# Kernel optimization log

Hardware: AMD Instinct MI355X
Metric: run time of the kernel (lower is better)

Reference implementation:

```python
import jax, jax.numpy as jnp
import numpy as np

B, S, D_IN, D_H = 4, 2048, 1024, 1024


def setup_inputs() -> dict:
    key = jax.random.key(0)
    k1, k2, k3, k4, k5, k6 = jax.random.split(key, 6)
    seq1 = jax.random.normal(k1, (B, S, D_IN), dtype=jnp.float32)
    seq2 = jax.random.normal(k2, (B, S, D_IN), dtype=jnp.float32)
    attn_mask = jax.random.randint(k3, (B, S, S), 0, 2).astype(jnp.bool_)
    # nn.Linear weights: shape [out, in], y = x @ W^T
    scale = 1.0 / np.sqrt(D_IN)
    Wq = jax.random.uniform(k4, (D_H, D_IN), dtype=jnp.float32, minval=-scale, maxval=scale)
    Wk = jax.random.uniform(k5, (D_H, D_IN), dtype=jnp.float32, minval=-scale, maxval=scale)
    Wv = jax.random.uniform(k6, (D_H, D_IN), dtype=jnp.float32, minval=-scale, maxval=scale)
    return {"seq1": seq1, "seq2": seq2, "attn_mask": attn_mask, "Wq": Wq, "Wk": Wk, "Wv": Wv}


def reference(seq1, seq2, attn_mask, Wq, Wk, Wv):
    q = jnp.einsum('bsd,hd->bsh', seq1, Wq)
    k = jnp.einsum('bsd,hd->bsh', seq2, Wk)
    v = jnp.einsum('bsd,hd->bsh', seq2, Wv)
    score = jnp.einsum('bqh,bkh->bqk', q, k) / jnp.sqrt(jnp.float32(q.shape[-1]))
    # faithful to torch.masked_fill(..., value=1e-09): masked positions set to 1e-9
    mask_score = jnp.where(attn_mask, jnp.float32(1e-09), score)
    # faithful to torch.softmax(..., dim=1): softmax over the QUERY axis
    score_matrix = jax.nn.softmax(mask_score, axis=1)
    out = jnp.einsum('bqk,bkh->bqh', score_matrix, v)
    return out
```

## Files before the change

### kernel.cpp

```cpp
#include <hip/hip_runtime.h>

typedef __bf16 bx8 __attribute__((ext_vector_type(8)));
typedef __bf16 bx4 __attribute__((ext_vector_type(4)));
typedef float  fx4 __attribute__((ext_vector_type(4)));
typedef unsigned long long u64;
typedef unsigned char u8;

#define B_   4
#define S_   2048
#define DIN  1024
#define DH   1024

#define MB ((size_t)1 << 20)
#define WS_A1 ((size_t)0)
#define WS_A2 ((size_t)16*MB)
#define WS_PU ((size_t)0)
#define WS_WQ ((size_t)32*MB)
#define WS_BM ((size_t)38*MB)
#define WS_Q  ((size_t)40*MB)
#define WS_K  ((size_t)56*MB)
#define WS_VT ((size_t)72*MB)
#define WS_CS ((size_t)88*MB)

__global__ void prep(const float* __restrict__ s1, const float* __restrict__ s2,
                     const float* __restrict__ wq, const float* __restrict__ wk,
                     const float* __restrict__ wv, const int* __restrict__ mask,
                     __bf16* __restrict__ o1, __bf16* __restrict__ o2,
                     __bf16* __restrict__ ow, u8* __restrict__ bm) {
  const int b = blockIdx.x;
  if (b < 9728) {
    const float* in;
    __bf16* out;
    size_t i;
    if (b < 8192) {
      in  = b < 4096 ? s1 : s2;
      out = b < 4096 ? o1 : o2;
      i = (size_t)(b & 4095) * 256 + threadIdx.x;
    } else {
      int g = b - 8192;
      in  = g < 512 ? wq : (g < 1024 ? wk : wv);
      out = ow + (size_t)(g >> 9) * (DH * DIN);
      i = (size_t)(g & 511) * 256 + threadIdx.x;
    }
    fx4 lo = ((const fx4*)in)[2 * i];
    fx4 hi = ((const fx4*)in)[2 * i + 1];
    bx8 o;
#pragma unroll
    for (int j = 0; j < 4; j++) { o[j] = (__bf16)lo[j]; o[j + 4] = (__bf16)hi[j]; }
    ((bx8*)out)[i] = o;
  } else {
    const int g = b - 9728;
    const int tid = threadIdx.x;
#pragma unroll
    for (int i = 0; i < 8; i++) {
      const int4* mp = (const int4*)mask + (((size_t)g * 16384 + (size_t)i * 2048) >> 2) + tid * 2;
      int4 v0 = mp[0], v1 = mp[1];
      unsigned byte = 0;
      byte |= (v0.x != 0);
      byte |= (v0.y != 0) << 1;
      byte |= (v0.z != 0) << 2;
      byte |= (v0.w != 0) << 3;
      byte |= (v1.x != 0) << 4;
      byte |= (v1.y != 0) << 5;
      byte |= (v1.z != 0) << 6;
      byte |= (v1.w != 0) << 7;
      bm[(size_t)g * 2048 + i * 256 + tid] = (u8)byte;
    }
  }
}


enum { EP_QKV = 0, EP_EXP = 2, EP_F32 = 3 };

#define GLD(gp, lp)                                                              \
  __builtin_amdgcn_global_load_lds(                                              \
      (const __attribute__((address_space(1))) void*)(const void*)(gp),          \
      (__attribute__((address_space(3))) void*)(void*)(lp), 16, 0, 0)

#define ENDSYNC()                                          \
  do {                                                     \
    asm volatile("s_waitcnt vmcnt(0)" ::: "memory");       \
    __builtin_amdgcn_s_barrier();                          \
    __builtin_amdgcn_sched_barrier(0);                     \
  } while (0)

#define MM(m, n, av, bv) \
  acc[m][n] = __builtin_amdgcn_mfma_f32_16x16x32_bf16(av, bv, acc[m][n], 0, 0, 0)

#define LDA_(bo, m, kk) (*(const bx8*)(aBase + (bo) + (m) * 2048 + ((kk) ? c1s : c0s)))
#define LDB_(bo, n, kk) (*(const bx8*)(bBase + (bo) + (n) * 2048 + ((kk) ? c1s : c0s)))

#define STAGE_A(kt, bo) do {                                              \
  GLD(pA + (kt),                    smem + (bo) + tid * 16);              \
  GLD(pA + (size_t)64 * K + (kt),   smem + (bo) + 8192 + tid * 16);       \
} while (0)
#define STAGE_B(kt, bo) do {                                              \
  GLD(pB + (kt),                    smem + (bo) + 16384 + tid * 16);      \
  GLD(pB + (size_t)64 * K + (kt),   smem + (bo) + 24576 + tid * 16);      \
} while (0)

template <int EPI>
__global__ __launch_bounds__(512, 4) void gemm128(
    const __bf16* __restrict__ A, const __bf16* __restrict__ Bm,
    void* __restrict__ Cout, void* __restrict__ Cout2,
    const void* __restrict__ Xtra, int N, int K, long sA, long sB) {
  extern __shared__ char smem[];

  int brow, bcol, bz = 0, qrow = 0;
  bool isQ = false;
  if (EPI == EP_QKV) {
    int f = (blockIdx.x & 7) * 192 + (blockIdx.x >> 3);
    if (f < 512) {
      isQ = true;
      qrow = (f >> 3) * 128;
      brow = qrow;
      bcol = (f & 7) * 128;
    } else {
      int g = f - 512;
      qrow = (g >> 4) * 128;
      brow = 8192 + qrow;
      bcol = (g & 15) * 128;
    }
  } else {
    const unsigned gx = gridDim.x, gy = gridDim.y;
    const unsigned nwg = gx * gy * gridDim.z;
    unsigned flat = (blockIdx.z * gy + blockIdx.y) * gx + blockIdx.x;
    flat = (flat & 7) * (nwg >> 3) + (flat >> 3);
    const int lx = __builtin_ctz(gx), ly = __builtin_ctz(gy);
    brow = ((flat >> lx) & (gy - 1)) * 128;
    bcol = (flat & (gx - 1)) * 128;
    bz   = flat >> (lx + ly);
    A  += (long)bz * sA;
    Bm += (long)bz * sB;
  }

  const int tid  = threadIdx.x;
  const int wid  = tid >> 6;
  const int lane = tid & 63;
  const int wr = wid >> 2;
  const int wc = wid & 3;

  fx4 acc[4][2] = {};

  const int gcol = (((tid & 7) ^ ((tid >> 3) & 7)) << 3);
  const __bf16* Bsel = (EPI == EP_QKV && !isQ) ? (Bm + (size_t)1048576) : Bm;
  const __bf16* pA = A    + (size_t)(brow + (tid >> 3)) * K + gcol;
  const __bf16* pB = Bsel + (size_t)(bcol + (tid >> 3)) * K + gcol;

  const int frow = lane & 15;
  const int slot = (lane >> 4) << 4;
  const int c0s  = slot ^ ((frow & 7) << 4);
  const int c1s  = (64 + slot) ^ ((frow & 7) << 4);
  const char* aBase = smem + (wr * 64 + frow) * 128;
  const char* bBase = smem + 16384 + (wc * 32 + frow) * 128;

  STAGE_A(0, 0); STAGE_B(0, 0);
  ENDSYNC();

  const int nt = K >> 6;
  int cur = 0, nb = 32768;
  bx8 a00, a01, a02, a03, a10, a11, a12, a13, b00, b01, b10, b11;

  for (int t = 0; t < nt; ++t) {
    const int k1 = (t + 1 < nt) ? (t + 1) * 64 : 0;

    STAGE_A(k1, nb); STAGE_B(k1, nb);

    a00 = LDA_(cur, 0, 0); a01 = LDA_(cur, 1, 0); a02 = LDA_(cur, 2, 0); a03 = LDA_(cur, 3, 0);
    b00 = LDB_(cur, 0, 0); b01 = LDB_(cur, 1, 0);
    a10 = LDA_(cur, 0, 1); a11 = LDA_(cur, 1, 1); a12 = LDA_(cur, 2, 1); a13 = LDA_(cur, 3, 1);
    b10 = LDB_(cur, 0, 1); b11 = LDB_(cur, 1, 1);

    __builtin_amdgcn_s_setprio(1);
    MM(0, 0, a00, b00); MM(0, 1, a00, b01);
    MM(1, 0, a01, b00); MM(1, 1, a01, b01);
    MM(2, 0, a02, b00); MM(2, 1, a02, b01);
    MM(3, 0, a03, b00); MM(3, 1, a03, b01);
    MM(0, 0, a10, b10); MM(0, 1, a10, b11);
    MM(1, 0, a11, b10); MM(1, 1, a11, b11);
    MM(2, 0, a12, b10); MM(2, 1, a12, b11);
    MM(3, 0, a13, b10); MM(3, 1, a13, b11);
    __builtin_amdgcn_s_setprio(0);

    ENDSYNC();
    int tmp = cur; cur = nb; nb = tmp;
  }

  const int r0 = wr * 64 + (lane >> 4) * 4;
  const int c0 = wc * 32 + (lane & 15);

  if (EPI == EP_QKV) {
    if (isQ) {
      __bf16* Cq = (__bf16*)Cout;
#pragma unroll
      for (int m = 0; m < 4; m++) {
        int row = qrow + r0 + m * 16;
#pragma unroll
        for (int n = 0; n < 2; n++) {
          int col = bcol + c0 + n * 16;
#pragma unroll
          for (int j = 0; j < 4; j++)
            Cq[(size_t)(row + j) * 1024 + col] = (__bf16)acc[m][n][j];
        }
      }
    } else if (bcol < 1024) {
      __bf16* Ck = (__bf16*)Cout2;
#pragma unroll
      for (int m = 0; m < 4; m++) {
        int rr = qrow + r0 + m * 16;
#pragma unroll
        for (int n = 0; n < 2; n++) {
          int col = bcol + c0 + n * 16;
#pragma unroll
          for (int j = 0; j < 4; j++)
            Ck[(size_t)(rr + j) * 1024 + col] = (__bf16)acc[m][n][j];
        }
      }
    } else {
      __bf16* Cv = (__bf16*)Xtra;
#pragma unroll
      for (int m = 0; m < 4; m++) {
        int rr = qrow + r0 + m * 16;
        size_t bb = (size_t)(rr >> 11) << 21;
        int sidx = rr & 2047;
#pragma unroll
        for (int n = 0; n < 2; n++) {
          int col = bcol + c0 + n * 16 - 1024;
          bx4 tv;
#pragma unroll
          for (int j = 0; j < 4; j++) tv[j] = (__bf16)acc[m][n][j];
          *(bx4*)&Cv[bb + (size_t)col * S_ + sidx] = tv;
        }
      }
    }
  } else if (EPI == EP_EXP) {
    __bf16* C    = (__bf16*)Cout + (size_t)bz * ((size_t)S_ * S_);
    const u8* Wm = (const u8*)Xtra + (((size_t)bz * S_ * S_) >> 3);
    float csum0 = 0.f, csum1 = 0.f;
#pragma unroll
    for (int m = 0; m < 4; m++) {
      int row = brow + r0 + m * 16;
#pragma unroll
      for (int n = 0; n < 2; n++) {
        int col = bcol + c0 + n * 16;
        float cl = 0.f;
#pragma unroll
        for (int j = 0; j < 4; j++) {
          size_t idx = (size_t)(row + j) * S_ + col;
          bool mk = (Wm[idx >> 3] >> (idx & 7)) & 1;
          float p = mk ? 1.0f : __expf(acc[m][n][j] * 0.03125f);
          cl += p;
          C[idx] = (__bf16)p;
        }
        if (n == 0) csum0 += cl; else csum1 += cl;
      }
    }
    csum0 += __shfl_xor(csum0, 16); csum0 += __shfl_xor(csum0, 32);
    csum1 += __shfl_xor(csum1, 16); csum1 += __shfl_xor(csum1, 32);
    if (lane < 16) {
      float* csp = (float*)Cout2 + (size_t)bz * S_ + bcol + wc * 32 + lane;
      atomicAdd(csp, csum0);
      atomicAdd(csp + 16, csum1);
    }
  } else {
    float* C = (float*)Cout + (size_t)bz * ((size_t)S_ * DH);
#pragma unroll
    for (int m = 0; m < 4; m++) {
      int row = brow + r0 + m * 16;
#pragma unroll
      for (int n = 0; n < 2; n++) {
        int col = bcol + c0 + n * 16;
#pragma unroll
        for (int j = 0; j < 4; j++)
          C[(size_t)(row + j) * N + col] = acc[m][n][j];
      }
    }
  }
}

__global__ void scale_vt(__bf16* __restrict__ vT, const float* __restrict__ cs) {
  size_t i = (size_t)blockIdx.x * blockDim.x + threadIdx.x;
  size_t e = i * 8;
  int b = (int)(e >> 21);
  int k = (int)(e & (S_ - 1));
  bx8 v = ((bx8*)vT)[i];
  const float* c = cs + (size_t)b * S_ + k;
#pragma unroll
  for (int j = 0; j < 8; j++) v[j] = (__bf16)((float)v[j] / c[j]);
  ((bx8*)vT)[i] = v;
}

extern "C" void kernel_launch(void* const* d_in, const int* in_sizes, int n_in,
                              void* d_out, int out_size, void* d_ws, size_t ws_size,
                              hipStream_t stream) {
  const float* seq1 = (const float*)d_in[0];
  const float* seq2 = (const float*)d_in[1];
  const int*   mask = (const int*)d_in[2];
  const float* Wq   = (const float*)d_in[3];
  const float* Wk   = (const float*)d_in[4];
  const float* Wv   = (const float*)d_in[5];

  char* ws = (char*)d_ws;
  __bf16* A1  = (__bf16*)(ws + WS_A1);
  __bf16* A2  = (__bf16*)(ws + WS_A2);
  __bf16* Pu  = (__bf16*)(ws + WS_PU);
  __bf16* WQb = (__bf16*)(ws + WS_WQ);
  u8*     bm  = (u8*)(ws + WS_BM);
  __bf16* qb  = (__bf16*)(ws + WS_Q);
  __bf16* kb  = (__bf16*)(ws + WS_K);
  __bf16* vTb = (__bf16*)(ws + WS_VT);
  float*  cs  = (float*)(ws + WS_CS);

  (void)hipFuncSetAttribute((const void*)gemm128<EP_QKV>,
      hipFuncAttributeMaxDynamicSharedMemorySize, 65536);
  (void)hipFuncSetAttribute((const void*)gemm128<EP_EXP>,
      hipFuncAttributeMaxDynamicSharedMemorySize, 65536);
  (void)hipFuncSetAttribute((const void*)gemm128<EP_F32>,
      hipFuncAttributeMaxDynamicSharedMemorySize, 65536);

  prep<<<10752, 256, 0, stream>>>(seq1, seq2, Wq, Wk, Wv, mask, A1, A2, WQb, bm);
  hipMemsetAsync(ws + WS_CS, 0, (size_t)B_ * S_ * sizeof(float), stream);

  gemm128<EP_QKV><<<1536, 512, 65536, stream>>>(
      A1, WQb, qb, kb, vTb, 0, DIN, 0, 0);

  gemm128<EP_EXP><<<dim3(S_ / 128, S_ / 128, B_), 512, 65536, stream>>>(
      qb, kb, Pu, cs, bm, S_, DH, (long)S_ * DH, (long)S_ * DH);

  scale_vt<<<(B_ * DH * S_ / 8) / 256, 256, 0, stream>>>(vTb, cs);

  gemm128<EP_F32><<<dim3(DH / 128, S_ / 128, B_), 512, 65536, stream>>>(
      Pu, vTb, (float*)d_out, nullptr, nullptr, DH, S_, (long)S_ * S_, (long)DH * S_);
}
```

Measured before the change: 164.7 us.

## Move mask bit-packing into QKV GEMM launch and fold column-sum zeroing into prep

Mask-to-bitmask packing moves out of the prep kernel and into extra blocks interleaved with the QKV projection GEMM, two packing blocks for every three GEMM tiles. The intent is for the bandwidth-bound mask read to overlap with the compute-bound GEMM. The separate hipMemsetAsync for the column-sum buffer is replaced by one extra prep block that zeroes it, which removes a launch. The cost is that the GEMM grid grows to 2560 blocks, and the lightweight mask blocks share launch slots and resources sized for the GEMM's 512 threads and 64KB LDS.

```diff
diff --git a/kernel.cpp b/kernel.cpp
--- a/kernel.cpp
+++ b/kernel.cpp
@@ -24,49 +24,36 @@
 
 __global__ void prep(const float* __restrict__ s1, const float* __restrict__ s2,
                      const float* __restrict__ wq, const float* __restrict__ wk,
-                     const float* __restrict__ wv, const int* __restrict__ mask,
+                     const float* __restrict__ wv,
                      __bf16* __restrict__ o1, __bf16* __restrict__ o2,
-                     __bf16* __restrict__ ow, u8* __restrict__ bm) {
+                     __bf16* __restrict__ ow, float* __restrict__ cs) {
   const int b = blockIdx.x;
-  if (b < 9728) {
-    const float* in;
-    __bf16* out;
-    size_t i;
-    if (b < 8192) {
-      in  = b < 4096 ? s1 : s2;
-      out = b < 4096 ? o1 : o2;
-      i = (size_t)(b & 4095) * 256 + threadIdx.x;
-    } else {
-      int g = b - 8192;
-      in  = g < 512 ? wq : (g < 1024 ? wk : wv);
-      out = ow + (size_t)(g >> 9) * (DH * DIN);
-      i = (size_t)(g & 511) * 256 + threadIdx.x;
-    }
-    fx4 lo = ((const fx4*)in)[2 * i];
-    fx4 hi = ((const fx4*)in)[2 * i + 1];
-    bx8 o;
-#pragma unroll
-    for (int j = 0; j < 4; j++) { o[j] = (__bf16)lo[j]; o[j + 4] = (__bf16)hi[j]; }
-    ((bx8*)out)[i] = o;
+  if (b >= 9728) {
+    ((fx4*)cs)[(threadIdx.x & 255) * 8 + (threadIdx.x >> 8)] = fx4{0.f, 0.f, 0.f, 0.f};
+#pragma unroll
+    for (int j = 1; j < 8; j++)
+      ((fx4*)cs)[(threadIdx.x & 255) * 8 + j] = fx4{0.f, 0.f, 0.f, 0.f};
+    return;
+  }
+  const float* in;
+  __bf16* out;
+  size_t i;
+  if (b < 8192) {
+    in  = b < 4096 ? s1 : s2;
+    out = b < 4096 ? o1 : o2;
+    i = (size_t)(b & 4095) * 256 + threadIdx.x;
   } else {
-    const int g = b - 9728;
-    const int tid = threadIdx.x;
-#pragma unroll
-    for (int i = 0; i < 8; i++) {
-      const int4* mp = (const int4*)mask + (((size_t)g * 16384 + (size_t)i * 2048) >> 2) + tid * 2;
-      int4 v0 = mp[0], v1 = mp[1];
-      unsigned byte = 0;
-      byte |= (v0.x != 0);
-      byte |= (v0.y != 0) << 1;
-      byte |= (v0.z != 0) << 2;
-      byte |= (v0.w != 0) << 3;
-      byte |= (v1.x != 0) << 4;
-      byte |= (v1.y != 0) << 5;
-      byte |= (v1.z != 0) << 6;
-      byte |= (v1.w != 0) << 7;
-      bm[(size_t)g * 2048 + i * 256 + tid] = (u8)byte;
-    }
-  }
+    int g = b - 8192;
+    in  = g < 512 ? wq : (g < 1024 ? wk : wv);
+    out = ow + (size_t)(g >> 9) * (DH * DIN);
+    i = (size_t)(g & 511) * 256 + threadIdx.x;
+  }
+  fx4 lo = ((const fx4*)in)[2 * i];
+  fx4 hi = ((const fx4*)in)[2 * i + 1];
+  bx8 o;
+#pragma unroll
+  for (int j = 0; j < 4; j++) { o[j] = (__bf16)lo[j]; o[j + 4] = (__bf16)hi[j]; }
+  ((bx8*)out)[i] = o;
 }
 
 
@@ -103,13 +90,37 @@
 __global__ __launch_bounds__(512, 4) void gemm128(
     const __bf16* __restrict__ A, const __bf16* __restrict__ Bm,
     void* __restrict__ Cout, void* __restrict__ Cout2,
-    const void* __restrict__ Xtra, int N, int K, long sA, long sB) {
+    const void* __restrict__ Xtra, const int* __restrict__ Msk,
+    u8* __restrict__ Bmo, int N, int K, long sA, long sB) {
   extern __shared__ char smem[];
 
   int brow, bcol, bz = 0, qrow = 0;
   bool isQ = false;
   if (EPI == EP_QKV) {
-    int f = (blockIdx.x & 7) * 192 + (blockIdx.x >> 3);
+    const int bid = blockIdx.x;
+    const int q5 = bid / 5, r5 = bid % 5;
+    if (r5 < 2) {
+      const int g = q5 * 2 + r5;
+      const int t = threadIdx.x;
+#pragma unroll
+      for (int i = 0; i < 4; i++) {
+        const int4* mp = (const int4*)Msk + (((size_t)g * 16384 + (size_t)i * 4096) >> 2) + t * 2;
+        int4 v0 = mp[0], v1 = mp[1];
+        unsigned byte = 0;
+        byte |= (v0.x != 0);
+        byte |= (v0.y != 0) << 1;
+        byte |= (v0.z != 0) << 2;
+        byte |= (v0.w != 0) << 3;
+        byte |= (v1.x != 0) << 4;
+        byte |= (v1.y != 0) << 5;
+        byte |= (v1.z != 0) << 6;
+        byte |= (v1.w != 0) << 7;
+        Bmo[(size_t)g * 2048 + i * 512 + t] = (u8)byte;
+      }
+      return;
+    }
+    const int gg = q5 * 3 + (r5 - 2);
+    const int f = (gg & 7) * 192 + (gg >> 3);
     if (f < 512) {
       isQ = true;
       qrow = (f >> 3) * 128;
@@ -318,17 +329,17 @@
   (void)hipFuncSetAttribute((const void*)gemm128<EP_F32>,
       hipFuncAttributeMaxDynamicSharedMemorySize, 65536);
 
-  prep<<<10752, 256, 0, stream>>>(seq1, seq2, Wq, Wk, Wv, mask, A1, A2, WQb, bm);
-  hipMemsetAsync(ws + WS_CS, 0, (size_t)B_ * S_ * sizeof(float), stream);
-
-  gemm128<EP_QKV><<<1536, 512, 65536, stream>>>(
-      A1, WQb, qb, kb, vTb, 0, DIN, 0, 0);
+  prep<<<9729, 256, 0, stream>>>(seq1, seq2, Wq, Wk, Wv, A1, A2, WQb, cs);
+
+  gemm128<EP_QKV><<<2560, 512, 65536, stream>>>(
+      A1, WQb, qb, kb, vTb, mask, bm, 0, DIN, 0, 0);
 
   gemm128<EP_EXP><<<dim3(S_ / 128, S_ / 128, B_), 512, 65536, stream>>>(
-      qb, kb, Pu, cs, bm, S_, DH, (long)S_ * DH, (long)S_ * DH);
+      qb, kb, Pu, cs, bm, nullptr, nullptr, S_, DH, (long)S_ * DH, (long)S_ * DH);
 
   scale_vt<<<(B_ * DH * S_ / 8) / 256, 256, 0, stream>>>(vTb, cs);
 
   gemm128<EP_F32><<<dim3(DH / 128, S_ / 128, B_), 512, 65536, stream>>>(
-      Pu, vTb, (float*)d_out, nullptr, nullptr, DH, S_, (long)S_ * S_, (long)DH * S_);
+      Pu, vTb, (float*)d_out, nullptr, nullptr, nullptr, nullptr, DH, S_,
+      (long)S_ * S_, (long)DH * S_);
 }
```

New measurement: 174.0 us. 1.06x slower.
